# Kernel optimization log

Measured on AMD Instinct MI355X. Metric: run time of the kernel, lower is better.

## Reference

```python
import jax, jax.numpy as jnp
import numpy as np

DIM = 1024
H = 16
D = DIM // H
B = 4
N = 1024
SUPPRESS = 0.1
SCALE = D ** -0.5


def setup_inputs() -> dict:
    key = jax.random.key(0)
    ks = jax.random.split(key, 16)
    s = 0.02
    inp = {
        "x": jax.random.normal(ks[0], (B, N, DIM), jnp.float32),
        "padding_mask": jax.random.randint(ks[1], (B, N), 0, 2).astype(bool),
        "alibi_bias": jax.random.normal(ks[2], (1, H, N, N), jnp.float32),
        "Wq": jax.random.normal(ks[3], (DIM, DIM), jnp.float32) * s,
        "bq": jnp.zeros((DIM,), jnp.float32),
        "Wk": jax.random.normal(ks[4], (DIM, DIM), jnp.float32) * s,
        "bk": jnp.zeros((DIM,), jnp.float32),
        "Wv": jax.random.normal(ks[5], (DIM, DIM), jnp.float32) * s,
        "bv": jnp.zeros((DIM,), jnp.float32),
        "WqC": jax.random.normal(ks[6], (D, D), jnp.float32) * s,
        "WAC": jax.random.normal(ks[7], (D, D), jnp.float32) * s,
        "bC": jax.random.normal(ks[8], (D,), jnp.float32) * s,
        "Wqg": jax.random.normal(ks[9], (D, D), jnp.float32) * s,
        "WAg": jax.random.normal(ks[10], (D, D), jnp.float32) * s,
        "bg": jax.random.normal(ks[11], (D,), jnp.float32) * s,
        "Wo": jax.random.normal(ks[12], (DIM, DIM), jnp.float32) * s,
        "bo": jnp.zeros((DIM,), jnp.float32),
    }
    return inp


def reference(x, padding_mask, alibi_bias, Wq, bq, Wk, bk, Wv, bv,
              WqC, WAC, bC, Wqg, WAg, bg, Wo, bo):
    Bx, Nx, C = x.shape
    # QKV projections -> [B, H, N, D]
    q = (x @ Wq.T + bq).reshape(Bx, Nx, H, D).transpose(0, 2, 1, 3)
    k = (x @ Wk.T + bk).reshape(Bx, Nx, H, D).transpose(0, 2, 1, 3)
    v = (x @ Wv.T + bv).reshape(Bx, Nx, H, D).transpose(0, 2, 1, 3)
    # scores [B, H, N, N] with alibi then key padding mask
    scores = jnp.einsum("bhnd,bhmd->bhnm", q * SCALE, k)
    scores = scores + alibi_bias  # alibi covers all H heads, broadcasts over B
    scores = jnp.where(padding_mask[:, None, None, :], -jnp.inf, scores)
    attn = jax.nn.softmax(scores.astype(jnp.float32), axis=-1).astype(q.dtype)
    A = jnp.einsum("bhnm,bhmd->bhnd", attn, v)
    # per-head gated linear fusion (W_* are D x D, shared across heads)
    C2 = jnp.einsum("bhnd,ed->bhne", q, WqC) + jnp.einsum("bhnd,ed->bhne", A, WAC) + bC
    g = jax.nn.sigmoid(jnp.einsum("bhnd,ed->bhne", q, Wqg) + jnp.einsum("bhnd,ed->bhne", A, WAg) + bg)
    G = (jnp.exp(g) + 1.0) * SUPPRESS
    Aega = G * C2  # [B, H, N, D]
    out = Aega.transpose(0, 2, 1, 3).reshape(Bx, Nx, C)
    return out @ Wo.T + bo
```

## Files before the change

kernel.cpp:

```cpp
#include <hip/hip_runtime.h>
#include <stdint.h>
#include <stddef.h>

#define SEQ   1024
#define CD    1024
#define NHD   16
#define HDD   64
#define NBB   4

typedef unsigned short u16t;
typedef __attribute__((ext_vector_type(4))) float f32x4;
typedef __attribute__((ext_vector_type(4))) unsigned int u32x4;
typedef __attribute__((ext_vector_type(8))) _Float16 f16x8;
typedef __attribute__((ext_vector_type(4))) unsigned short u16x4;

__device__ __forceinline__ u16t f2h(float f) {
  _Float16 h = (_Float16)f;
  return __builtin_bit_cast(u16t, h);
}

__device__ __forceinline__ f32x4 MFMA(u32x4 a, u32x4 b, f32x4 c) {
  return __builtin_amdgcn_mfma_f32_16x16x32_f16(
      __builtin_bit_cast(f16x8, a), __builtin_bit_cast(f16x8, b), c, 0, 0, 0);
}

__device__ __forceinline__ void gl_lds16(const u16t* g, u16t* l) {
  __builtin_amdgcn_global_load_lds(
      (const __attribute__((address_space(1))) unsigned int*)g,
      (__attribute__((address_space(3))) unsigned int*)l, 16, 0, 0);
}

struct ConvArgs {
  const float* src[9];
  u16t* dst[9];
  int n[9];
};

__global__ void conv_kernel(ConvArgs a) {
  const int tid = blockIdx.x * blockDim.x + threadIdx.x;
  const int nth = gridDim.x * blockDim.x;
  for (int s = 0; s < 9; ++s) {
    const float4* src = (const float4*)a.src[s];
    u16x4* dst = (u16x4*)a.dst[s];
    const int n4 = a.n[s] >> 2;
    for (int i = tid; i < n4; i += nth) {
      float4 f = src[i];
      u16x4 o = { f2h(f.x), f2h(f.y), f2h(f.z), f2h(f.w) };
      dst[i] = o;
    }
  }
}

__global__ void mask_prep_kernel(const void* __restrict__ mask,
                                 float* __restrict__ maskbias) {
  __shared__ int notI32, notU8;
  if (threadIdx.x == 0) { notI32 = 0; notU8 = 0; }
  __syncthreads();
  const unsigned int* mi = (const unsigned int*)mask;
  const unsigned char* mb = (const unsigned char*)mask;
  int nI = 0, nU = 0;
  for (int i = threadIdx.x; i < 1024; i += 256) {
    if (mi[i] > 1u) nI = 1;
  }
  for (int i = threadIdx.x; i < 4096; i += 256) {
    if (mb[i] > 1) nU = 1;
  }
  if (nI) atomicOr(&notI32, 1);
  if (nU) atomicOr(&notU8, 1);
  __syncthreads();
  const int mode = (!notI32) ? 0 : ((!notU8) ? 1 : 2);
  for (int i = threadIdx.x; i < NBB * SEQ; i += 256) {
    bool m;
    if (mode == 0)      m = mi[i] != 0u;
    else if (mode == 1) m = mb[i] != 0;
    else                m = ((const float*)mask)[i] != 0.0f;
    maskbias[i] = m ? -1e30f : 0.0f;
  }
}

template <int MODE>
__global__ __launch_bounds__(256, 2) void gemm_kernel(
    const u16t* __restrict__ A,
    const u16t* __restrict__ B0, const u16t* __restrict__ B1,
    const u16t* __restrict__ B2,
    const float* __restrict__ bias0, const float* __restrict__ bias1,
    const float* __restrict__ bias2,
    void* __restrict__ out0, void* __restrict__ out1, void* __restrict__ out2) {
  __shared__ alignas(16) u16t As[128 * 32];
  __shared__ alignas(16) u16t Bs[128 * 32];

  const int tid = threadIdx.x;
  const int m0 = blockIdx.x * 128;
  int n0, mat = 0;
  const u16t* Bsel;
  const float* biassel;
  if constexpr (MODE == 0) {
    mat = (int)blockIdx.y >> 3;
    n0 = ((int)blockIdx.y & 7) * 128;
    Bsel = (mat == 0) ? B0 : ((mat == 1) ? B1 : B2);
    biassel = (mat == 0) ? bias0 : ((mat == 1) ? bias1 : bias2);
  } else {
    n0 = (int)blockIdx.y * 128;
    Bsel = B0;
    biassel = bias0;
  }

  const int wid = tid >> 6, lane = tid & 63;
  const int l16 = lane & 15, lq = lane >> 4;
  const int wr = (wid >> 1) * 64, wc = (wid & 1) * 64;

  const int srow = lane >> 2;
  const int scol = (lane & 3) * 8;
  const u16t* Ag = A + (size_t)(m0 + wid * 32 + srow) * CD + scol;
  const u16t* Bg = Bsel + (size_t)(n0 + wid * 32 + srow) * CD + scol;
  u16t* AsW = &As[(wid * 32 + srow) * 32 + scol];
  u16t* BsW = &Bs[(wid * 32 + srow) * 32 + scol];

  f32x4 acc[4][4] = {};

  for (int k0 = 0; k0 < CD; k0 += 32) {
    __syncthreads();
    gl_lds16(Ag + k0, AsW);
    gl_lds16(Ag + k0 + (size_t)16 * CD, AsW + 16 * 32);
    gl_lds16(Bg + k0, BsW);
    gl_lds16(Bg + k0 + (size_t)16 * CD, BsW + 16 * 32);
    __syncthreads();
    u32x4 af[4], bf[4];
#pragma unroll
    for (int i = 0; i < 4; ++i) {
      af[i] = *(const u32x4*)(&As[(wr + i * 16 + l16) * 32 + lq * 8]);
      bf[i] = *(const u32x4*)(&Bs[(wc + i * 16 + l16) * 32 + lq * 8]);
    }
#pragma unroll
    for (int i = 0; i < 4; ++i)
#pragma unroll
      for (int j = 0; j < 4; ++j)
        acc[i][j] = MFMA(af[i], bf[j], acc[i][j]);
  }

  if constexpr (MODE == 1) {
    float* outp = (float*)out0;
#pragma unroll
    for (int i = 0; i < 4; ++i) {
#pragma unroll
      for (int j = 0; j < 4; ++j) {
        const int col = n0 + wc + j * 16 + l16;
        const float bb = biassel[col];
#pragma unroll
        for (int r = 0; r < 4; ++r) {
          const int row = m0 + wr + i * 16 + lq * 4 + r;
          outp[(size_t)row * CD + col] = acc[i][j][r] + bb;
        }
      }
    }
  } else {
    u16t* outp = (mat == 0) ? (u16t*)out0 : ((mat == 1) ? (u16t*)out1 : (u16t*)out2);
#pragma unroll
    for (int i = 0; i < 4; ++i) {
#pragma unroll
      for (int j = 0; j < 4; ++j) {
        const int cl = n0 + wc + j * 16 + l16;
        const int hh = cl >> 6, dd = cl & 63;
        const float bb = biassel[cl];
#pragma unroll
        for (int r = 0; r < 4; ++r) {
          const int row = m0 + wr + i * 16 + lq * 4 + r;
          const int bidx = row >> 10, nidx = row & 1023;
          if (mat == 2) {
            outp[(((size_t)(bidx * NHD + hh)) * HDD + dd) * SEQ + nidx] =
                f2h(acc[i][j][r] + bb);
          } else {
            outp[(((size_t)(bidx * NHD + hh)) * SEQ + nidx) * HDD + dd] =
                f2h(acc[i][j][r] + bb);
          }
        }
      }
    }
  }
}

__global__ __launch_bounds__(256, 3) void attn_kernel(
    const u16t* __restrict__ Q, const u16t* __restrict__ K,
    const u16t* __restrict__ VT, const float* __restrict__ alibi,
    const float* __restrict__ maskbias, u16t* __restrict__ Aout) {
  __shared__ alignas(16) u16t Ks[64][72];
  __shared__ alignas(16) u16t Vts[64][72];

  const int qt = blockIdx.x, h = blockIdx.y, b = blockIdx.z;
  const int tid = threadIdx.x, wid = tid >> 6, lane = tid & 63;
  const int l16 = lane & 15, lq = lane >> 4;
  const size_t hoff = ((size_t)(b * NHD + h)) * SEQ * HDD;
  const int q0 = qt * 64 + wid * 16;
  const float* al = alibi + (size_t)h * SEQ * SEQ + (size_t)(q0 + l16) * SEQ;
  const float* mb = maskbias + b * SEQ;

  const u32x4 qf0 = *(const u32x4*)(Q + hoff + (size_t)(q0 + l16) * HDD + lq * 8);
  const u32x4 qf1 = *(const u32x4*)(Q + hoff + (size_t)(q0 + l16) * HDD + 32 + lq * 8);

  f32x4 Oacc[4] = {};
  float mrow = -1e30f, lrow = 0.f;

  const int sr = tid >> 2;
  const int sc = (tid & 3) * 16;
  const u16t* Kg = K + hoff + (size_t)sr * HDD + sc;
  const u16t* Vg = VT + hoff + (size_t)sr * SEQ + sc;

  u32x4 kv0 = *(const u32x4*)(Kg);
  u32x4 kv1 = *(const u32x4*)(Kg + 8);
  u32x4 vv0 = *(const u32x4*)(Vg);
  u32x4 vv1 = *(const u32x4*)(Vg + 8);
  f32x4 ali[2][4];
#pragma unroll
  for (int kt = 0; kt < 4; ++kt)
    ali[0][kt] = *(const f32x4*)(al + kt * 16 + lq * 4);

#pragma unroll 2
  for (int t = 0; t < 16; ++t) {
    const int k0 = t * 64;
    const int tc = t & 1, tn = (t + 1) & 1;
    asm volatile("" ::: "memory");
    __builtin_amdgcn_s_barrier();
    asm volatile("" ::: "memory");
    *(u32x4*)(&Ks[sr][sc]) = kv0;
    *(u32x4*)(&Ks[sr][sc + 8]) = kv1;
    *(u32x4*)(&Vts[sr][sc]) = vv0;
    *(u32x4*)(&Vts[sr][sc + 8]) = vv1;
    {
      const int kn = (t < 15) ? (k0 + 64) : 0;
      kv0 = *(const u32x4*)(Kg + (size_t)kn * HDD);
      kv1 = *(const u32x4*)(Kg + (size_t)kn * HDD + 8);
      vv0 = *(const u32x4*)(Vg + kn);
      vv1 = *(const u32x4*)(Vg + kn + 8);
    }
    asm volatile("s_waitcnt lgkmcnt(0)" ::: "memory");
    __builtin_amdgcn_s_barrier();
    asm volatile("" ::: "memory");

    {
      const float* aln = al + ((t < 15) ? (k0 + 64) : 0);
#pragma unroll
      for (int kt = 0; kt < 4; ++kt)
        ali[tn][kt] = *(const f32x4*)(aln + kt * 16 + lq * 4);
    }

    f32x4 s[4];
#pragma unroll
    for (int kt = 0; kt < 4; ++kt) {
      u32x4 kf0 = *(const u32x4*)(&Ks[kt * 16 + l16][lq * 8]);
      u32x4 kf1 = *(const u32x4*)(&Ks[kt * 16 + l16][32 + lq * 8]);
      f32x4 z = {};
      z = MFMA(kf0, qf0, z);
      z = MFMA(kf1, qf1, z);
      s[kt] = z;
    }
#pragma unroll
    for (int kt = 0; kt < 4; ++kt) {
      const f32x4 a4 = ali[tc][kt];
      const f32x4 m4 = *(const f32x4*)(mb + k0 + kt * 16 + lq * 4);
#pragma unroll
      for (int r = 0; r < 4; ++r)
        s[kt][r] = s[kt][r] * 0.125f + a4[r] + m4[r];
    }
    float mx = s[0][0];
#pragma unroll
    for (int kt = 0; kt < 4; ++kt)
#pragma unroll
      for (int r = 0; r < 4; ++r) mx = fmaxf(mx, s[kt][r]);
    mx = fmaxf(mx, __shfl_xor(mx, 16, 64));
    mx = fmaxf(mx, __shfl_xor(mx, 32, 64));
    const float mnew = fmaxf(mrow, mx);
    const float corr = __expf(mrow - mnew);
    mrow = mnew;
    float ps = 0.f;
#pragma unroll
    for (int kt = 0; kt < 4; ++kt)
#pragma unroll
      for (int r = 0; r < 4; ++r) {
        const float p = __expf(s[kt][r] - mnew);
        s[kt][r] = p;
        ps += p;
      }
    ps += __shfl_xor(ps, 16, 64);
    ps += __shfl_xor(ps, 32, 64);
    lrow = lrow * corr + ps;
#pragma unroll
    for (int r = 0; r < 4; ++r) {
      const float cr = __shfl(corr, lq * 4 + r, 64);
      Oacc[0][r] *= cr; Oacc[1][r] *= cr; Oacc[2][r] *= cr; Oacc[3][r] *= cr;
    }
    unsigned int wp[4][2];
#pragma unroll
    for (int kt = 0; kt < 4; ++kt) {
      wp[kt][0] = (unsigned)f2h(s[kt][0]) | ((unsigned)f2h(s[kt][1]) << 16);
      wp[kt][1] = (unsigned)f2h(s[kt][2]) | ((unsigned)f2h(s[kt][3]) << 16);
    }
#pragma unroll
    for (int ks = 0; ks < 2; ++ks) {
      u32x4 pa;
#pragma unroll
      for (int m = 0; m < 4; ++m) {
        const int srcl = l16 + ((lq & 1) << 5) + ((m >> 1) << 4);
        const unsigned lo = __shfl(wp[ks * 2][m & 1], srcl, 64);
        const unsigned hi = __shfl(wp[ks * 2 + 1][m & 1], srcl, 64);
        pa[m] = (lq & 2) ? hi : lo;
      }
#pragma unroll
      for (int dt = 0; dt < 4; ++dt) {
        u32x4 vf = *(const u32x4*)(&Vts[dt * 16 + l16][ks * 32 + lq * 8]);
        Oacc[dt] = MFMA(pa, vf, Oacc[dt]);
      }
    }
  }

#pragma unroll
  for (int r = 0; r < 4; ++r) {
    const float linv = 1.0f / __shfl(lrow, lq * 4 + r, 64);
    const int qr = q0 + lq * 4 + r;
#pragma unroll
    for (int dt = 0; dt < 4; ++dt)
      Aout[hoff + (size_t)qr * HDD + dt * 16 + l16] = f2h(Oacc[dt][r] * linv);
  }
}

__global__ __launch_bounds__(256, 2) void fuse_kernel(
    const u16t* __restrict__ Q, const u16t* __restrict__ Aatt,
    const u16t* __restrict__ W4, const float* __restrict__ bC,
    const float* __restrict__ bg, u16t* __restrict__ Aega) {
  __shared__ alignas(16) u16t Ws[4][64][72];
  const int tid = threadIdx.x;
  for (int i = tid; i < 2048; i += 256) {
    const int w = i >> 9;
    const int r = (i >> 3) & 63;
    const int c = (i & 7) * 8;
    *(u32x4*)(&Ws[w][r][c]) = *(const u32x4*)(W4 + (size_t)(w * 64 + r) * 64 + c);
  }
  __syncthreads();
  const int wid = tid >> 6, lane = tid & 63;
  const int l16 = lane & 15, lq = lane >> 4;
  const size_t row0 = (size_t)blockIdx.x * 64 + wid * 16;

  const u32x4 qf0 = *(const u32x4*)(Q + (row0 + l16) * HDD + lq * 8);
  const u32x4 qf1 = *(const u32x4*)(Q + (row0 + l16) * HDD + 32 + lq * 8);
  const u32x4 af0 = *(const u32x4*)(Aatt + (row0 + l16) * HDD + lq * 8);
  const u32x4 af1 = *(const u32x4*)(Aatt + (row0 + l16) * HDD + 32 + lq * 8);

#pragma unroll
  for (int et = 0; et < 4; ++et) {
    u32x4 wc0 = *(const u32x4*)(&Ws[0][et * 16 + l16][lq * 8]);
    u32x4 wc1 = *(const u32x4*)(&Ws[0][et * 16 + l16][32 + lq * 8]);
    u32x4 wa0 = *(const u32x4*)(&Ws[1][et * 16 + l16][lq * 8]);
    u32x4 wa1 = *(const u32x4*)(&Ws[1][et * 16 + l16][32 + lq * 8]);
    u32x4 wg0 = *(const u32x4*)(&Ws[2][et * 16 + l16][lq * 8]);
    u32x4 wg1 = *(const u32x4*)(&Ws[2][et * 16 + l16][32 + lq * 8]);
    u32x4 wh0 = *(const u32x4*)(&Ws[3][et * 16 + l16][lq * 8]);
    u32x4 wh1 = *(const u32x4*)(&Ws[3][et * 16 + l16][32 + lq * 8]);
    f32x4 c2 = {};
    c2 = MFMA(qf0, wc0, c2);
    c2 = MFMA(qf1, wc1, c2);
    c2 = MFMA(af0, wa0, c2);
    c2 = MFMA(af1, wa1, c2);
    f32x4 gg = {};
    gg = MFMA(qf0, wg0, gg);
    gg = MFMA(qf1, wg1, gg);
    gg = MFMA(af0, wh0, gg);
    gg = MFMA(af1, wh1, gg);
    const int e = et * 16 + l16;
    const float bCe = bC[e], bge = bg[e];
#pragma unroll
    for (int r = 0; r < 4; ++r) {
      const size_t row = row0 + lq * 4 + r;
      const int bidx = (int)(row >> 14);
      const int hh = (int)((row >> 10) & 15);
      const int nn = (int)(row & 1023);
      const float C2v = c2[r] + bCe;
      const float gv = 1.f / (1.f + __expf(-(gg[r] + bge)));
      const float Gv = (__expf(gv) + 1.f) * 0.1f;
      Aega[((size_t)(bidx * SEQ + nn)) * CD + hh * 64 + e] = f2h(Gv * C2v);
    }
  }
}

static constexpr size_t OFF_X16 = 0;
static constexpr size_t OFF_WQ  = 8388608;
static constexpr size_t OFF_WK  = 10485760;
static constexpr size_t OFF_WV  = 12582912;
static constexpr size_t OFF_WO  = 14680064;
static constexpr size_t OFF_W4  = 16777216;
static constexpr size_t OFF_MB  = 16809984;
static constexpr size_t OFF_Q   = 16826368;
static constexpr size_t OFF_K   = 25214976;
static constexpr size_t OFF_V   = 33603584;
static constexpr size_t OFF_A   = 41992192;
static constexpr size_t OFF_AEG = 50380800;

extern "C" void kernel_launch(void* const* d_in, const int* in_sizes, int n_in,
                              void* d_out, int out_size, void* d_ws, size_t ws_size,
                              hipStream_t stream) {
  const float* x     = (const float*)d_in[0];
  const void*  pmask = d_in[1];
  const float* alibi = (const float*)d_in[2];
  const float* Wq    = (const float*)d_in[3];
  const float* bq    = (const float*)d_in[4];
  const float* Wk    = (const float*)d_in[5];
  const float* bk    = (const float*)d_in[6];
  const float* Wv    = (const float*)d_in[7];
  const float* bv    = (const float*)d_in[8];
  const float* WqC   = (const float*)d_in[9];
  const float* WAC   = (const float*)d_in[10];
  const float* bC    = (const float*)d_in[11];
  const float* Wqg   = (const float*)d_in[12];
  const float* WAg   = (const float*)d_in[13];
  const float* bg    = (const float*)d_in[14];
  const float* Wo    = (const float*)d_in[15];
  const float* bo    = (const float*)d_in[16];

  char* w = (char*)d_ws;
  u16t* X16 = (u16t*)(w + OFF_X16);
  u16t* WQp = (u16t*)(w + OFF_WQ);
  u16t* WKp = (u16t*)(w + OFF_WK);
  u16t* WVp = (u16t*)(w + OFF_WV);
  u16t* WOp = (u16t*)(w + OFF_WO);
  u16t* W4p = (u16t*)(w + OFF_W4);
  float* MBp = (float*)(w + OFF_MB);
  u16t* Qb  = (u16t*)(w + OFF_Q);
  u16t* Kb  = (u16t*)(w + OFF_K);
  u16t* VTb = (u16t*)(w + OFF_V);
  u16t* Ab  = (u16t*)(w + OFF_A);
  u16t* AEG = (u16t*)(w + OFF_AEG);

  ConvArgs ca;
  ca.src[0] = x;   ca.dst[0] = X16;            ca.n[0] = 4 * 1024 * 1024;
  ca.src[1] = Wq;  ca.dst[1] = WQp;            ca.n[1] = 1024 * 1024;
  ca.src[2] = Wk;  ca.dst[2] = WKp;            ca.n[2] = 1024 * 1024;
  ca.src[3] = Wv;  ca.dst[3] = WVp;            ca.n[3] = 1024 * 1024;
  ca.src[4] = Wo;  ca.dst[4] = WOp;            ca.n[4] = 1024 * 1024;
  ca.src[5] = WqC; ca.dst[5] = W4p;            ca.n[5] = 4096;
  ca.src[6] = WAC; ca.dst[6] = W4p + 4096;     ca.n[6] = 4096;
  ca.src[7] = Wqg; ca.dst[7] = W4p + 8192;     ca.n[7] = 4096;
  ca.src[8] = WAg; ca.dst[8] = W4p + 12288;    ca.n[8] = 4096;

  hipLaunchKernelGGL(conv_kernel, dim3(1024), dim3(256), 0, stream, ca);
  hipLaunchKernelGGL(mask_prep_kernel, dim3(1), dim3(256), 0, stream, pmask, MBp);
  hipLaunchKernelGGL(HIP_KERNEL_NAME(gemm_kernel<0>), dim3(32, 24), dim3(256), 0,
                     stream, X16, WQp, WKp, WVp, bq, bk, bv,
                     (void*)Qb, (void*)Kb, (void*)VTb);
  hipLaunchKernelGGL(attn_kernel, dim3(16, 16, 4), dim3(256), 0, stream,
                     Qb, Kb, VTb, alibi, MBp, Ab);
  hipLaunchKernelGGL(fuse_kernel, dim3(1024), dim3(256), 0, stream,
                     Qb, Ab, W4p, bC, bg, AEG);
  hipLaunchKernelGGL(HIP_KERNEL_NAME(gemm_kernel<1>), dim3(32, 8), dim3(256), 0,
                     stream, AEG, WOp, (const u16t*)nullptr, (const u16t*)nullptr,
                     bo, (const float*)nullptr, (const float*)nullptr,
                     d_out, (void*)nullptr, (void*)nullptr);
}
```

Before: 162.4 us.

## Transpose PV MFMA output, drop alibi double buffer, raise attention occupancy

The attention kernel swaps the operands of the P·V MFMA so each lane's accumulator rows match the lane's own query row. That removes the per-row shuffles for the softmax correction and the final normalisation. The alibi prefetch goes from a two-slot register buffer to a single slot reloaded right after use, and launch bounds rise from 3 to 4 blocks per CU to cut register pressure and raise occupancy. The output is now staged through LDS for coalesced 16-byte stores, and P is packed to fp16 with cvt_pkrtz (round toward zero), which slightly changes rounding. The prefetched alibi has less time to arrive before its next use, and the tighter register budget may cause spills.

```diff
diff --git a/kernel.cpp b/kernel.cpp
--- a/kernel.cpp
+++ b/kernel.cpp
@@ -12,6 +12,7 @@
 typedef __attribute__((ext_vector_type(4))) float f32x4;
 typedef __attribute__((ext_vector_type(4))) unsigned int u32x4;
 typedef __attribute__((ext_vector_type(8))) _Float16 f16x8;
+typedef __attribute__((ext_vector_type(2))) _Float16 f16x2;
 typedef __attribute__((ext_vector_type(4))) unsigned short u16x4;
 
 __device__ __forceinline__ u16t f2h(float f) {
@@ -179,7 +180,7 @@
   }
 }
 
-__global__ __launch_bounds__(256, 3) void attn_kernel(
+__global__ __launch_bounds__(256, 4) void attn_kernel(
     const u16t* __restrict__ Q, const u16t* __restrict__ K,
     const u16t* __restrict__ VT, const float* __restrict__ alibi,
     const float* __restrict__ maskbias, u16t* __restrict__ Aout) {
@@ -209,15 +210,14 @@
   u32x4 kv1 = *(const u32x4*)(Kg + 8);
   u32x4 vv0 = *(const u32x4*)(Vg);
   u32x4 vv1 = *(const u32x4*)(Vg + 8);
-  f32x4 ali[2][4];
+  f32x4 ali[4];
 #pragma unroll
   for (int kt = 0; kt < 4; ++kt)
-    ali[0][kt] = *(const f32x4*)(al + kt * 16 + lq * 4);
+    ali[kt] = *(const f32x4*)(al + kt * 16 + lq * 4);
 
 #pragma unroll 2
   for (int t = 0; t < 16; ++t) {
     const int k0 = t * 64;
-    const int tc = t & 1, tn = (t + 1) & 1;
     asm volatile("" ::: "memory");
     __builtin_amdgcn_s_barrier();
     asm volatile("" ::: "memory");
@@ -236,13 +236,6 @@
     __builtin_amdgcn_s_barrier();
     asm volatile("" ::: "memory");
 
-    {
-      const float* aln = al + ((t < 15) ? (k0 + 64) : 0);
-#pragma unroll
-      for (int kt = 0; kt < 4; ++kt)
-        ali[tn][kt] = *(const f32x4*)(aln + kt * 16 + lq * 4);
-    }
-
     f32x4 s[4];
 #pragma unroll
     for (int kt = 0; kt < 4; ++kt) {
@@ -255,12 +248,19 @@
     }
 #pragma unroll
     for (int kt = 0; kt < 4; ++kt) {
-      const f32x4 a4 = ali[tc][kt];
+      const f32x4 a4 = ali[kt];
       const f32x4 m4 = *(const f32x4*)(mb + k0 + kt * 16 + lq * 4);
 #pragma unroll
       for (int r = 0; r < 4; ++r)
         s[kt][r] = s[kt][r] * 0.125f + a4[r] + m4[r];
     }
+    {
+      const float* aln = al + ((t < 15) ? (k0 + 64) : 0);
+#pragma unroll
+      for (int kt = 0; kt < 4; ++kt)
+        ali[kt] = *(const f32x4*)(aln + kt * 16 + lq * 4);
+    }
+
     float mx = s[0][0];
 #pragma unroll
     for (int kt = 0; kt < 4; ++kt)
@@ -284,15 +284,17 @@
     ps += __shfl_xor(ps, 32, 64);
     lrow = lrow * corr + ps;
 #pragma unroll
-    for (int r = 0; r < 4; ++r) {
-      const float cr = __shfl(corr, lq * 4 + r, 64);
-      Oacc[0][r] *= cr; Oacc[1][r] *= cr; Oacc[2][r] *= cr; Oacc[3][r] *= cr;
-    }
+    for (int dt = 0; dt < 4; ++dt)
+#pragma unroll
+      for (int r = 0; r < 4; ++r) Oacc[dt][r] *= corr;
+
     unsigned int wp[4][2];
 #pragma unroll
     for (int kt = 0; kt < 4; ++kt) {
-      wp[kt][0] = (unsigned)f2h(s[kt][0]) | ((unsigned)f2h(s[kt][1]) << 16);
-      wp[kt][1] = (unsigned)f2h(s[kt][2]) | ((unsigned)f2h(s[kt][3]) << 16);
+      wp[kt][0] = __builtin_bit_cast(unsigned int,
+                    __builtin_amdgcn_cvt_pkrtz(s[kt][0], s[kt][1]));
+      wp[kt][1] = __builtin_bit_cast(unsigned int,
+                    __builtin_amdgcn_cvt_pkrtz(s[kt][2], s[kt][3]));
     }
 #pragma unroll
     for (int ks = 0; ks < 2; ++ks) {
@@ -307,18 +309,25 @@
 #pragma unroll
       for (int dt = 0; dt < 4; ++dt) {
         u32x4 vf = *(const u32x4*)(&Vts[dt * 16 + l16][ks * 32 + lq * 8]);
-        Oacc[dt] = MFMA(pa, vf, Oacc[dt]);
+        Oacc[dt] = MFMA(vf, pa, Oacc[dt]);
       }
     }
   }
 
-#pragma unroll
-  for (int r = 0; r < 4; ++r) {
-    const float linv = 1.0f / __shfl(lrow, lq * 4 + r, 64);
-    const int qr = q0 + lq * 4 + r;
+  __syncthreads();
+  {
+    const float linv = 1.0f / lrow;
 #pragma unroll
     for (int dt = 0; dt < 4; ++dt)
-      Aout[hoff + (size_t)qr * HDD + dt * 16 + l16] = f2h(Oacc[dt][r] * linv);
+#pragma unroll
+      for (int r = 0; r < 4; ++r)
+        Ks[wid * 16 + l16][dt * 16 + lq * 4 + r] = f2h(Oacc[dt][r] * linv);
+    const int qr = q0 - wid * 16 + (wid * 16 + (lane >> 2));
+    const int cc = (lane & 3) * 16;
+    u32x4 o0 = *(const u32x4*)(&Ks[wid * 16 + (lane >> 2)][cc]);
+    u32x4 o1 = *(const u32x4*)(&Ks[wid * 16 + (lane >> 2)][cc + 8]);
+    *(u32x4*)(Aout + hoff + (size_t)qr * HDD + cc) = o0;
+    *(u32x4*)(Aout + hoff + (size_t)qr * HDD + cc + 8) = o1;
   }
 }
 
```

Result: faster. 157.1 us (-3.3%).
